# Optimization experiments

Measured on AMD Instinct MI355X. Metric: run time of the kernel, lower is better.

The kernel has to match this reference:

```python
import jax, jax.numpy as jnp
import numpy as np

BN_EPS = 1e-5


def _bn(x, gamma, beta):
    # training-mode BatchNorm1d: biased batch stats over the edge/batch axis
    mean = jnp.mean(x, axis=0, keepdims=True)
    var = jnp.mean((x - mean) ** 2, axis=0, keepdims=True)
    return (x - mean) * jax.lax.rsqrt(var + BN_EPS) * gamma + beta


def setup_inputs() -> dict:
    key = jax.random.key(0)
    ks = jax.random.split(key, 20)
    N, E = 20000, 300000
    in_drug, in_prot, hidden = 256, 512, 256
    h2 = 2 * hidden

    def u(k, shape, fan_in):
        b = 1.0 / np.sqrt(fan_in)
        return jax.random.uniform(k, shape, jnp.float32, -b, b)

    return {
        "x_drug": jax.random.normal(ks[0], (N, in_drug), jnp.float32),
        "x_prot": jax.random.normal(ks[1], (N, in_prot), jnp.float32),
        "edge_index": jax.random.randint(ks[2], (2, E), 0, N, jnp.int64),
        "W_src": u(ks[3], (hidden, in_drug), in_drug),
        "W_dst": u(ks[4], (hidden, in_prot), in_prot),
        "W_gate": u(ks[5], (h2, h2), h2),
        "b_gate": u(ks[6], (h2,), h2),
        "W1": u(ks[7], (hidden, h2), h2),
        "b1": u(ks[8], (hidden,), h2),
        "g1": jnp.ones((hidden,), jnp.float32),
        "be1": jnp.zeros((hidden,), jnp.float32),
        "W2": u(ks[9], (hidden, hidden), hidden),
        "b2": u(ks[10], (hidden,), hidden),
        "g2": jnp.ones((hidden,), jnp.float32),
        "be2": jnp.zeros((hidden,), jnp.float32),
        "W3": u(ks[11], (1, hidden), hidden),
        "b3": u(ks[12], (1,), hidden),
        "W_bil": u(ks[13], (1, hidden, hidden), hidden),
        "b_bil": u(ks[14], (1,), hidden),
    }


def reference(x_drug, x_prot, edge_index, W_src, W_dst, W_gate, b_gate,
              W1, b1, g1, be1, W2, b2, g2, be2, W3, b3, W_bil, b_bil):
    src, dst = edge_index[0], edge_index[1]
    h_src = x_drug[src] @ W_src.T            # [E, H]
    h_dst = x_prot[dst] @ W_dst.T            # [E, H]
    h_cat = jnp.concatenate([h_src, h_dst], axis=1)  # [E, 2H]
    gate = jax.nn.sigmoid(h_cat @ W_gate.T + b_gate)
    h = gate * h_cat
    # MLP (dropout is identity here)
    h1 = jax.nn.relu(_bn(h @ W1.T + b1, g1, be1))
    h2_ = jax.nn.relu(_bn(h1 @ W2.T + b2, g2, be2))
    mlp_score = (h2_ @ W3.T + b3).reshape(-1)
    # Bilinear: out_ek = sum_ij h_src_ei W_kij h_dst_ej + b_k
    bil_score = (jnp.einsum("ei,kij,ej->ek", h_src, W_bil, h_dst) + b_bil).reshape(-1)
    return mlp_score + bil_score
```

## Files before the change

kernel.cpp:

```cpp
#include <hip/hip_runtime.h>
#include <hip/hip_bf16.h>

typedef unsigned short u16;
typedef __attribute__((ext_vector_type(8))) short bf16x8;
typedef __attribute__((ext_vector_type(8))) unsigned short us8;
typedef __attribute__((ext_vector_type(4))) float f32x4;


__device__ __forceinline__ float b2f(u16 u) {
    union { unsigned u32; float f; } x; x.u32 = ((unsigned)u) << 16; return x.f;
}
__device__ __forceinline__ u16 f2b(float f) {
    union { float f; unsigned u; } x; x.f = f;
    unsigned r = x.u + 0x7fffu + ((x.u >> 16) & 1u);
    return (u16)(r >> 16);
}

__global__ __launch_bounds__(256) void zero_kernel(float* p, int n) {
    int i = blockIdx.x * 256 + threadIdx.x;
    if (i < n) p[i] = 0.f;
}

__global__ __launch_bounds__(256) void cvt_kernel(const float* __restrict__ in,
                                                  u16* __restrict__ out, int n4) {
    int i = blockIdx.x * 256 + threadIdx.x;
    const int stride = gridDim.x * 256;
    for (; i < n4; i += stride) {
        float4 v = ((const float4*)in)[i];
        ushort4 o; o.x = f2b(v.x); o.y = f2b(v.y); o.z = f2b(v.z); o.w = f2b(v.w);
        ((ushort4*)out)[i] = o;
    }
}

#define OP_PLAIN  0
#define OP_GATE   1
#define OP_BNRELU 2

template <int AOP, bool STATS, bool BIAS>
__global__ __launch_bounds__(256, 2) void mfma_gemm(
    const u16* __restrict__ Ain, int lda,
    const u16* __restrict__ Wb, int ldb,
    u16* __restrict__ C, int ldc,
    int M, int K,
    const int* __restrict__ ei, int E,
    const u16* __restrict__ Gs, const u16* __restrict__ Gd,
    const u16* __restrict__ Hs, const u16* __restrict__ Hd,
    const float* __restrict__ scaleK, const float* __restrict__ shiftK,
    const float* __restrict__ bias,
    float* __restrict__ sums)
{
    __shared__ u16 As[128][72];
    __shared__ u16 Bs[256][72];
    __shared__ float wsum[2][2][256];
    __shared__ int sx[128], dx[128];

    const int t = threadIdx.x;
    const int row0 = blockIdx.x * 128;
    const int col0 = blockIdx.y * 256;

    if constexpr (AOP == OP_GATE) {
        if (t < 128) {
            const int e = min(row0 + t, M - 1);
            sx[t] = ei[e]; dx[t] = ei[E + e];
        }
        __syncthreads();
    }

    const int arow = t >> 1;
    const int ks = (t & 1) * 32;
    const int agr = min(row0 + arow, M - 1);

    const int w = t >> 6, lane = t & 63;
    const int wr = w >> 1, wc = w & 1;
    const int lrow = lane & 15, lkg = lane >> 4;

    f32x4 acc[4][8] = {};

    for (int k0 = 0; k0 < K; k0 += 64) {
        {
            const u16* wp = Wb + (size_t)(col0 + t) * ldb + k0;
#pragma unroll
            for (int q = 0; q < 8; ++q)
                *(us8*)&Bs[t][q * 8] = *(const us8*)(wp + q * 8);
        }
        if constexpr (AOP == OP_PLAIN) {
            const u16* ap = Ain + (size_t)agr * lda + k0 + ks;
#pragma unroll
            for (int q = 0; q < 4; ++q)
                *(us8*)&As[arow][ks + q * 8] = *(const us8*)(ap + q * 8);
        } else if constexpr (AOP == OP_GATE) {
            const int s = sx[arow], d = dx[arow];
            const u16* gsp = Gs + (size_t)s * 512 + k0 + ks;
            const u16* gdp = Gd + (size_t)d * 512 + k0 + ks;
            const u16* hp = (k0 < 256) ? (Hs + (size_t)s * 256 + k0 + ks)
                                       : (Hd + (size_t)d * 256 + (k0 - 256) + ks);
#pragma unroll
            for (int q = 0; q < 4; ++q) {
                us8 g8 = *(const us8*)(gsp + q * 8);
                us8 d8 = *(const us8*)(gdp + q * 8);
                us8 h8 = *(const us8*)(hp + q * 8);
                us8 o;
#pragma unroll
                for (int j = 0; j < 8; ++j) {
                    const float x = b2f(g8[j]) + b2f(d8[j]);
                    const float g = 1.f / (1.f + __expf(-x));
                    o[j] = f2b(g * b2f(h8[j]));
                }
                *(us8*)&As[arow][ks + q * 8] = o;
            }
        } else {
            const u16* ap = Ain + (size_t)agr * lda + k0 + ks;
#pragma unroll
            for (int q = 0; q < 4; ++q) {
                us8 a8 = *(const us8*)(ap + q * 8);
                us8 o;
#pragma unroll
                for (int j = 0; j < 8; ++j) {
                    const int k = k0 + ks + q * 8 + j;
                    o[j] = f2b(fmaxf(fmaf(b2f(a8[j]), scaleK[k], shiftK[k]), 0.f));
                }
                *(us8*)&As[arow][ks + q * 8] = o;
            }
        }
        __syncthreads();
#pragma unroll
        for (int kk = 0; kk < 64; kk += 32) {
            bf16x8 af[4];
#pragma unroll
            for (int mi = 0; mi < 4; ++mi)
                af[mi] = *(const bf16x8*)&As[wr * 64 + mi * 16 + lrow][kk + lkg * 8];
#pragma unroll
            for (int ni = 0; ni < 8; ++ni) {
                bf16x8 bfr = *(const bf16x8*)&Bs[wc * 128 + ni * 16 + lrow][kk + lkg * 8];
#pragma unroll
                for (int mi = 0; mi < 4; ++mi)
                    acc[mi][ni] = __builtin_amdgcn_mfma_f32_16x16x32_bf16(
                        af[mi], bfr, acc[mi][ni], 0, 0, 0);
            }
        }
        __syncthreads();
    }

#pragma unroll
    for (int ni = 0; ni < 8; ++ni) {
        const int gcol = col0 + wc * 128 + ni * 16 + lrow;
        const float bv = BIAS ? bias[gcol] : 0.f;
        float s = 0.f, ss = 0.f;
#pragma unroll
        for (int mi = 0; mi < 4; ++mi) {
            f32x4 v = acc[mi][ni];
#pragma unroll
            for (int j = 0; j < 4; ++j) {
                const int grow = row0 + wr * 64 + mi * 16 + lkg * 4 + j;
                const float x = v[j] + bv;
                if (grow < M) {
                    C[(size_t)grow * ldc + gcol] = f2b(x);
                    if (STATS) { s += x; ss = fmaf(x, x, ss); }
                }
            }
        }
        if constexpr (STATS) {
            s  += __shfl_xor(s, 16, 64);  s  += __shfl_xor(s, 32, 64);
            ss += __shfl_xor(ss, 16, 64); ss += __shfl_xor(ss, 32, 64);
            if (lkg == 0) {
                wsum[0][wr][wc * 128 + ni * 16 + lrow] = s;
                wsum[1][wr][wc * 128 + ni * 16 + lrow] = ss;
            }
        }
    }
    if constexpr (STATS) {
        __syncthreads();
        atomicAdd(&sums[t],       wsum[0][0][t] + wsum[0][1][t]);
        atomicAdd(&sums[256 + t], wsum[1][0][t] + wsum[1][1][t]);
    }
}

__global__ void finalize_kernel(
    const float* __restrict__ sums, const float* __restrict__ g,
    const float* __restrict__ be, int M,
    float* __restrict__ scale, float* __restrict__ shift)
{
    const int c = threadIdx.x;
    const float inv = 1.f / (float)M;
    const float mean = sums[c] * inv;
    const float var  = sums[256 + c] * inv - mean * mean;
    const float sc = g[c] * rsqrtf(var + 1e-5f);
    scale[c] = sc;
    shift[c] = fmaf(-mean, sc, be[c]);
}

__global__ __launch_bounds__(256) void final_kernel(
    const u16* __restrict__ Z2,
    const float* __restrict__ scale2, const float* __restrict__ shift2,
    const float* __restrict__ W3, const float* __restrict__ b3,
    const int* __restrict__ ei,
    const u16* __restrict__ Hs, const u16* __restrict__ Bd,
    const float* __restrict__ b_bil,
    float* __restrict__ out, int E)
{
    const int w = threadIdx.x >> 6, lane = threadIdx.x & 63;
    const int e = blockIdx.x * 4 + w;
    if (e >= E) return;
    const int s = ei[e], d = ei[E + e];
    ushort4 zv = *(const ushort4*)(Z2 + (size_t)e * 256 + lane * 4);
    ushort4 hv = *(const ushort4*)(Hs + (size_t)s * 256 + lane * 4);
    ushort4 bv = *(const ushort4*)(Bd + (size_t)d * 256 + lane * 4);
    float4 sc = *(const float4*)(scale2 + lane * 4);
    float4 sh = *(const float4*)(shift2 + lane * 4);
    float4 w3 = *(const float4*)(W3 + lane * 4);
    const u16 zq[4] = {zv.x, zv.y, zv.z, zv.w};
    const u16 hq[4] = {hv.x, hv.y, hv.z, hv.w};
    const u16 bq[4] = {bv.x, bv.y, bv.z, bv.w};
    const float scq[4] = {sc.x, sc.y, sc.z, sc.w};
    const float shq[4] = {sh.x, sh.y, sh.z, sh.w};
    const float wq[4] = {w3.x, w3.y, w3.z, w3.w};
    float acc = 0.f;
#pragma unroll
    for (int i = 0; i < 4; ++i) {
        const float x = fmaxf(fmaf(b2f(zq[i]), scq[i], shq[i]), 0.f);
        acc = fmaf(x, wq[i], acc);
        acc = fmaf(b2f(hq[i]), b2f(bq[i]), acc);
    }
#pragma unroll
    for (int off = 32; off; off >>= 1) acc += __shfl_down(acc, off, 64);
    if (lane == 0) out[e] = acc + b3[0] + b_bil[0];
}

extern "C" void kernel_launch(void* const* d_in, const int* in_sizes, int n_in,
                              void* d_out, int out_size, void* d_ws, size_t ws_size,
                              hipStream_t stream)
{
    const float* x_drug = (const float*)d_in[0];
    const float* x_prot = (const float*)d_in[1];
    const int*   ei     = (const int*)d_in[2];
    const float* W_src  = (const float*)d_in[3];
    const float* W_dst  = (const float*)d_in[4];
    const float* W_gate = (const float*)d_in[5];
    const float* b_gate = (const float*)d_in[6];
    const float* W1     = (const float*)d_in[7];
    const float* g1     = (const float*)d_in[9];
    const float* be1    = (const float*)d_in[10];
    const float* W2     = (const float*)d_in[11];
    const float* g2     = (const float*)d_in[13];
    const float* be2    = (const float*)d_in[14];
    const float* W3     = (const float*)d_in[15];
    const float* b3     = (const float*)d_in[16];
    const float* W_bil  = (const float*)d_in[17];
    const float* b_bil  = (const float*)d_in[18];
    float* out = (float*)d_out;

    const int N = in_sizes[0] / 256;
    const int E = in_sizes[2] / 2;

    char* wp_ = (char*)d_ws;
    auto alloc = [&](size_t bytes) {
        char* p = wp_; wp_ += (bytes + 255) & ~(size_t)255; return p;
    };
    u16* xdb    = (u16*)alloc((size_t)N * 256 * 2);
    u16* xpb    = (u16*)alloc((size_t)N * 512 * 2);
    u16* Wsrcb  = (u16*)alloc(256 * 256 * 2);
    u16* Wdstb  = (u16*)alloc(256 * 512 * 2);
    u16* Wgateb = (u16*)alloc(512 * 512 * 2);
    u16* Wbilb  = (u16*)alloc(256 * 256 * 2);
    u16* W1b    = (u16*)alloc(256 * 512 * 2);
    u16* W2b    = (u16*)alloc(256 * 256 * 2);
    u16* Hs     = (u16*)alloc((size_t)N * 256 * 2);
    u16* Hd     = (u16*)alloc((size_t)N * 256 * 2);
    u16* Gs     = (u16*)alloc((size_t)N * 512 * 2);
    u16* Gd     = (u16*)alloc((size_t)N * 512 * 2);
    u16* Bd     = (u16*)alloc((size_t)N * 256 * 2);
    u16* z      = (u16*)alloc((size_t)E * 256 * 2);
    float* sums   = (float*)alloc(1024 * 4);
    float* scale1 = (float*)alloc(256 * 4);
    float* shift1 = (float*)alloc(256 * 4);
    float* scale2 = (float*)alloc(256 * 4);
    float* shift2 = (float*)alloc(256 * 4);

    zero_kernel<<<4, 256, 0, stream>>>(sums, 1024);

    auto cvt = [&](const float* in, u16* o, int n) {
        const int n4 = n / 4;
        cvt_kernel<<<min((n4 + 255) / 256, 2048), 256, 0, stream>>>(in, o, n4);
    };
    cvt(x_drug, xdb, N * 256);
    cvt(x_prot, xpb, N * 512);
    cvt(W_src,  Wsrcb,  256 * 256);
    cvt(W_dst,  Wdstb,  256 * 512);
    cvt(W_gate, Wgateb, 512 * 512);
    cvt(W_bil,  Wbilb,  256 * 256);
    cvt(W1,     W1b,    256 * 512);
    cvt(W2,     W2b,    256 * 256);

    const int mbN = (N + 127) / 128;
    const int mbE = (E + 127) / 128;

#define NULLS nullptr, 0, nullptr, nullptr, nullptr, nullptr
    mfma_gemm<OP_PLAIN, false, false><<<dim3(mbN, 1), 256, 0, stream>>>(
        xdb, 256, Wsrcb, 256, Hs, 256, N, 256, NULLS, nullptr, nullptr, nullptr, nullptr);
    mfma_gemm<OP_PLAIN, false, false><<<dim3(mbN, 1), 256, 0, stream>>>(
        xpb, 512, Wdstb, 512, Hd, 256, N, 512, NULLS, nullptr, nullptr, nullptr, nullptr);
    mfma_gemm<OP_PLAIN, false, true><<<dim3(mbN, 2), 256, 0, stream>>>(
        Hs, 256, Wgateb, 512, Gs, 512, N, 256, NULLS, nullptr, nullptr, b_gate, nullptr);
    mfma_gemm<OP_PLAIN, false, false><<<dim3(mbN, 2), 256, 0, stream>>>(
        Hd, 256, Wgateb + 256, 512, Gd, 512, N, 256, NULLS, nullptr, nullptr, nullptr, nullptr);
    mfma_gemm<OP_PLAIN, false, false><<<dim3(mbN, 1), 256, 0, stream>>>(
        Hd, 256, Wbilb, 256, Bd, 256, N, 256, NULLS, nullptr, nullptr, nullptr, nullptr);

    mfma_gemm<OP_GATE, true, false><<<dim3(mbE, 1), 256, 0, stream>>>(
        nullptr, 0, W1b, 512, z, 256, E, 512,
        ei, E, Gs, Gd, Hs, Hd, nullptr, nullptr, nullptr, sums);
    finalize_kernel<<<1, 256, 0, stream>>>(sums, g1, be1, E, scale1, shift1);

    mfma_gemm<OP_BNRELU, true, false><<<dim3(mbE, 1), 256, 0, stream>>>(
        z, 256, W2b, 256, z, 256, E, 256,
        NULLS, scale1, shift1, nullptr, sums + 512);
    finalize_kernel<<<1, 256, 0, stream>>>(sums + 512, g2, be2, E, scale2, shift2);

    final_kernel<<<(E + 3) / 4, 256, 0, stream>>>(
        z, scale2, shift2, W3, b3, ei, Hs, Bd, b_bil, out, E);
#undef NULLS
}
```

Before: 636.6 us.

## Double-buffer GEMM tiles, batch node GEMMs, fuse input casts and bilinear dot

```diff
diff --git a/kernel.cpp b/kernel.cpp
--- a/kernel.cpp
+++ b/kernel.cpp
@@ -21,158 +21,285 @@
     if (i < n) p[i] = 0.f;
 }
 
-__global__ __launch_bounds__(256) void cvt_kernel(const float* __restrict__ in,
-                                                  u16* __restrict__ out, int n4) {
+struct CvtSeg { const float* in; u16* out; int n4; };
+struct CvtArr { CvtSeg s[6]; int tot4; };
+__global__ __launch_bounds__(256) void cvt_fused(CvtArr ca) {
     int i = blockIdx.x * 256 + threadIdx.x;
-    const int stride = gridDim.x * 256;
-    for (; i < n4; i += stride) {
-        float4 v = ((const float4*)in)[i];
-        ushort4 o; o.x = f2b(v.x); o.y = f2b(v.y); o.z = f2b(v.z); o.w = f2b(v.w);
-        ((ushort4*)out)[i] = o;
-    }
-}
-
-#define OP_PLAIN  0
-#define OP_GATE   1
-#define OP_BNRELU 2
-
-template <int AOP, bool STATS, bool BIAS>
-__global__ __launch_bounds__(256, 2) void mfma_gemm(
-    const u16* __restrict__ Ain, int lda,
-    const u16* __restrict__ Wb, int ldb,
-    u16* __restrict__ C, int ldc,
-    int M, int K,
-    const int* __restrict__ ei, int E,
-    const u16* __restrict__ Gs, const u16* __restrict__ Gd,
-    const u16* __restrict__ Hs, const u16* __restrict__ Hd,
-    const float* __restrict__ scaleK, const float* __restrict__ shiftK,
-    const float* __restrict__ bias,
-    float* __restrict__ sums)
+    if (i >= ca.tot4) return;
+    int k = 0, off = i;
+#pragma unroll
+    for (int q = 0; q < 6; ++q) {
+        if (off < ca.s[q].n4) { k = q; break; }
+        off -= ca.s[q].n4;
+    }
+    float4 v = ((const float4*)ca.s[k].in)[off];
+    ushort4 o; o.x = f2b(v.x); o.y = f2b(v.y); o.z = f2b(v.z); o.w = f2b(v.w);
+    ((ushort4*)ca.s[k].out)[off] = o;
+}
+
+struct GDesc {
+    const void* A; int lda; int a_f32;
+    const u16* W; int ldb;
+    u16* C; int ldc;
+    int K;
+    const float* bias;
+};
+template <int NY> struct GDescArr { GDesc d[NY]; };
+
+template <int NY>
+__global__ __launch_bounds__(256, 2) void mfma_node(GDescArr<NY> da, int M)
 {
-    __shared__ u16 As[128][72];
-    __shared__ u16 Bs[256][72];
-    __shared__ float wsum[2][2][256];
-    __shared__ int sx[128], dx[128];
-
+    const GDesc dd = da.d[blockIdx.y];
+    __shared__ u16 As[2][128][40];
+    __shared__ u16 Bs[2][256][40];
     const int t = threadIdx.x;
     const int row0 = blockIdx.x * 128;
-    const int col0 = blockIdx.y * 256;
-
-    if constexpr (AOP == OP_GATE) {
-        if (t < 128) {
-            const int e = min(row0 + t, M - 1);
-            sx[t] = ei[e]; dx[t] = ei[E + e];
-        }
-        __syncthreads();
-    }
-
-    const int arow = t >> 1;
-    const int ks = (t & 1) * 32;
+    const int arow = t >> 1, aks = (t & 1) * 16;
     const int agr = min(row0 + arow, M - 1);
-
     const int w = t >> 6, lane = t & 63;
     const int wr = w >> 1, wc = w & 1;
     const int lrow = lane & 15, lkg = lane >> 4;
+    const int NIT = dd.K >> 5;
 
     f32x4 acc[4][8] = {};
-
-    for (int k0 = 0; k0 < K; k0 += 64) {
-        {
-            const u16* wp = Wb + (size_t)(col0 + t) * ldb + k0;
-#pragma unroll
-            for (int q = 0; q < 8; ++q)
-                *(us8*)&Bs[t][q * 8] = *(const us8*)(wp + q * 8);
-        }
-        if constexpr (AOP == OP_PLAIN) {
-            const u16* ap = Ain + (size_t)agr * lda + k0 + ks;
-#pragma unroll
-            for (int q = 0; q < 4; ++q)
-                *(us8*)&As[arow][ks + q * 8] = *(const us8*)(ap + q * 8);
-        } else if constexpr (AOP == OP_GATE) {
-            const int s = sx[arow], d = dx[arow];
-            const u16* gsp = Gs + (size_t)s * 512 + k0 + ks;
-            const u16* gdp = Gd + (size_t)d * 512 + k0 + ks;
-            const u16* hp = (k0 < 256) ? (Hs + (size_t)s * 256 + k0 + ks)
-                                       : (Hd + (size_t)d * 256 + (k0 - 256) + ks);
-#pragma unroll
-            for (int q = 0; q < 4; ++q) {
-                us8 g8 = *(const us8*)(gsp + q * 8);
-                us8 d8 = *(const us8*)(gdp + q * 8);
-                us8 h8 = *(const us8*)(hp + q * 8);
+    us8 ar[2], br[4];
+    float4 fr[4];
+
+    auto load_regs = [&](int it) {
+        const int k0 = it << 5;
+        if (dd.a_f32) {
+            const float* ap = (const float*)dd.A + (size_t)agr * dd.lda + k0 + aks;
+#pragma unroll
+            for (int q = 0; q < 4; ++q) fr[q] = *(const float4*)(ap + q * 4);
+        } else {
+            const u16* ap = (const u16*)dd.A + (size_t)agr * dd.lda + k0 + aks;
+            ar[0] = *(const us8*)ap; ar[1] = *(const us8*)(ap + 8);
+        }
+        const u16* wp = dd.W + (size_t)t * dd.ldb + k0;
+#pragma unroll
+        for (int q = 0; q < 4; ++q) br[q] = *(const us8*)(wp + q * 8);
+    };
+    auto proc_write = [&](int b) {
+        if (dd.a_f32) {
+#pragma unroll
+            for (int q = 0; q < 2; ++q) {
                 us8 o;
-#pragma unroll
-                for (int j = 0; j < 8; ++j) {
-                    const float x = b2f(g8[j]) + b2f(d8[j]);
-                    const float g = 1.f / (1.f + __expf(-x));
-                    o[j] = f2b(g * b2f(h8[j]));
-                }
-                *(us8*)&As[arow][ks + q * 8] = o;
+                const float fq[8] = {fr[q*2].x, fr[q*2].y, fr[q*2].z, fr[q*2].w,
+                                     fr[q*2+1].x, fr[q*2+1].y, fr[q*2+1].z, fr[q*2+1].w};
+#pragma unroll
+                for (int j = 0; j < 8; ++j) o[j] = f2b(fq[j]);
+                *(us8*)&As[b][arow][aks + q * 8] = o;
             }
         } else {
-            const u16* ap = Ain + (size_t)agr * lda + k0 + ks;
-#pragma unroll
-            for (int q = 0; q < 4; ++q) {
-                us8 a8 = *(const us8*)(ap + q * 8);
-                us8 o;
-#pragma unroll
-                for (int j = 0; j < 8; ++j) {
-                    const int k = k0 + ks + q * 8 + j;
-                    o[j] = f2b(fmaxf(fmaf(b2f(a8[j]), scaleK[k], shiftK[k]), 0.f));
-                }
-                *(us8*)&As[arow][ks + q * 8] = o;
-            }
-        }
+            *(us8*)&As[b][arow][aks] = ar[0];
+            *(us8*)&As[b][arow][aks + 8] = ar[1];
+        }
+#pragma unroll
+        for (int q = 0; q < 4; ++q) *(us8*)&Bs[b][t][q * 8] = br[q];
+    };
+    auto do_mfma = [&](int b) {
+        bf16x8 af[4];
+#pragma unroll
+        for (int mi = 0; mi < 4; ++mi)
+            af[mi] = *(const bf16x8*)&As[b][wr * 64 + mi * 16 + lrow][lkg * 8];
+#pragma unroll
+        for (int ni = 0; ni < 8; ++ni) {
+            bf16x8 bfr = *(const bf16x8*)&Bs[b][wc * 128 + ni * 16 + lrow][lkg * 8];
+#pragma unroll
+            for (int mi = 0; mi < 4; ++mi)
+                acc[mi][ni] = __builtin_amdgcn_mfma_f32_16x16x32_bf16(
+                    af[mi], bfr, acc[mi][ni], 0, 0, 0);
+        }
+    };
+
+    load_regs(0); proc_write(0); __syncthreads();
+    for (int it = 0; it < NIT; ++it) {
+        const int cur = it & 1;
+        if (it + 1 < NIT) load_regs(it + 1);
+        do_mfma(cur);
+        if (it + 1 < NIT) proc_write(cur ^ 1);
         __syncthreads();
-#pragma unroll
-        for (int kk = 0; kk < 64; kk += 32) {
-            bf16x8 af[4];
-#pragma unroll
-            for (int mi = 0; mi < 4; ++mi)
-                af[mi] = *(const bf16x8*)&As[wr * 64 + mi * 16 + lrow][kk + lkg * 8];
-#pragma unroll
-            for (int ni = 0; ni < 8; ++ni) {
-                bf16x8 bfr = *(const bf16x8*)&Bs[wc * 128 + ni * 16 + lrow][kk + lkg * 8];
-#pragma unroll
-                for (int mi = 0; mi < 4; ++mi)
-                    acc[mi][ni] = __builtin_amdgcn_mfma_f32_16x16x32_bf16(
-                        af[mi], bfr, acc[mi][ni], 0, 0, 0);
-            }
-        }
-        __syncthreads();
     }
 
 #pragma unroll
     for (int ni = 0; ni < 8; ++ni) {
-        const int gcol = col0 + wc * 128 + ni * 16 + lrow;
-        const float bv = BIAS ? bias[gcol] : 0.f;
-        float s = 0.f, ss = 0.f;
+        const int gcol = wc * 128 + ni * 16 + lrow;
+        const float bv = dd.bias ? dd.bias[gcol] : 0.f;
 #pragma unroll
         for (int mi = 0; mi < 4; ++mi) {
             f32x4 v = acc[mi][ni];
 #pragma unroll
             for (int j = 0; j < 4; ++j) {
                 const int grow = row0 + wr * 64 + mi * 16 + lkg * 4 + j;
-                const float x = v[j] + bv;
-                if (grow < M) {
-                    C[(size_t)grow * ldc + gcol] = f2b(x);
-                    if (STATS) { s += x; ss = fmaf(x, x, ss); }
+                if (grow < M) dd.C[(size_t)grow * dd.ldc + gcol] = f2b(v[j] + bv);
+            }
+        }
+    }
+}
+
+#define OP_GATE   1
+#define OP_BNRELU 2
+
+template <int AOP>
+__global__ __launch_bounds__(256, 2) void mfma_edge(
+    const u16* __restrict__ Ain,
+    const u16* __restrict__ Wb, int ldb, int K,
+    u16* __restrict__ C, int E,
+    const int* __restrict__ ei,
+    const u16* __restrict__ Gs, const u16* __restrict__ Gd,
+    const u16* __restrict__ Hs, const u16* __restrict__ Hd,
+    const u16* __restrict__ Bd, const float* __restrict__ b_bil,
+    float* __restrict__ bil,
+    const float* __restrict__ scaleK, const float* __restrict__ shiftK,
+    float* __restrict__ sums)
+{
+    __shared__ u16 As[2][128][40];
+    __shared__ u16 Bs[2][256][40];
+    __shared__ float wsum[2][2][256];
+    __shared__ int sx[128], dx[128];
+
+    const int t = threadIdx.x;
+    const int row0 = blockIdx.x * 128;
+
+    if constexpr (AOP == OP_GATE) {
+        if (t < 128) {
+            const int e = min(row0 + t, E - 1);
+            sx[t] = ei[e]; dx[t] = ei[E + e];
+        }
+        __syncthreads();
+    }
+
+    const int arow = t >> 1, aks = (t & 1) * 16;
+    const int agr = min(row0 + arow, E - 1);
+    const int w = t >> 6, lane = t & 63;
+    const int wr = w >> 1, wc = w & 1;
+    const int lrow = lane & 15, lkg = lane >> 4;
+    const int NIT = K >> 5;
+
+    f32x4 acc[4][8] = {};
+    float bdot = 0.f;
+    us8 g1r[2], g2r[2], hr[2], bdr[2], br[4];
+    float4 scA[2], scB[2], shA[2], shB[2];
+
+    auto load_regs = [&](int it) {
+        const int k0 = it << 5;
+        const int kg = k0 + aks;
+        if constexpr (AOP == OP_GATE) {
+            const int s = sx[arow], d = dx[arow];
+            const u16* gsp = Gs + (size_t)s * 512 + kg;
+            const u16* gdp = Gd + (size_t)d * 512 + kg;
+            g1r[0] = *(const us8*)gsp; g1r[1] = *(const us8*)(gsp + 8);
+            g2r[0] = *(const us8*)gdp; g2r[1] = *(const us8*)(gdp + 8);
+            const u16* hp = (k0 < 256) ? (Hs + (size_t)s * 256 + kg)
+                                       : (Hd + (size_t)d * 256 + kg - 256);
+            hr[0] = *(const us8*)hp; hr[1] = *(const us8*)(hp + 8);
+            if (k0 < 256) {
+                const u16* bp = Bd + (size_t)dx[arow] * 256 + kg;
+                bdr[0] = *(const us8*)bp; bdr[1] = *(const us8*)(bp + 8);
+            }
+        } else {
+            const u16* ap = Ain + (size_t)agr * 256 + kg;
+            g1r[0] = *(const us8*)ap; g1r[1] = *(const us8*)(ap + 8);
+#pragma unroll
+            for (int q = 0; q < 2; ++q) {
+                scA[q] = *(const float4*)(scaleK + kg + q * 8);
+                scB[q] = *(const float4*)(scaleK + kg + q * 8 + 4);
+                shA[q] = *(const float4*)(shiftK + kg + q * 8);
+                shB[q] = *(const float4*)(shiftK + kg + q * 8 + 4);
+            }
+        }
+        const u16* wp = Wb + (size_t)t * ldb + k0;
+#pragma unroll
+        for (int q = 0; q < 4; ++q) br[q] = *(const us8*)(wp + q * 8);
+    };
+    auto proc_write = [&](int it, int b) {
+        const int k0 = it << 5;
+#pragma unroll
+        for (int q = 0; q < 2; ++q) {
+            us8 o;
+            if constexpr (AOP == OP_GATE) {
+#pragma unroll
+                for (int j = 0; j < 8; ++j) {
+                    const float x = b2f(g1r[q][j]) + b2f(g2r[q][j]);
+                    const float g = 1.f / (1.f + __expf(-x));
+                    o[j] = f2b(g * b2f(hr[q][j]));
                 }
-            }
-        }
-        if constexpr (STATS) {
-            s  += __shfl_xor(s, 16, 64);  s  += __shfl_xor(s, 32, 64);
-            ss += __shfl_xor(ss, 16, 64); ss += __shfl_xor(ss, 32, 64);
-            if (lkg == 0) {
-                wsum[0][wr][wc * 128 + ni * 16 + lrow] = s;
-                wsum[1][wr][wc * 128 + ni * 16 + lrow] = ss;
-            }
-        }
-    }
-    if constexpr (STATS) {
+                if (k0 < 256) {
+#pragma unroll
+                    for (int j = 0; j < 8; ++j)
+                        bdot = fmaf(b2f(hr[q][j]), b2f(bdr[q][j]), bdot);
+                }
+            } else {
+                const float scq[8] = {scA[q].x, scA[q].y, scA[q].z, scA[q].w,
+                                      scB[q].x, scB[q].y, scB[q].z, scB[q].w};
+                const float shq[8] = {shA[q].x, shA[q].y, shA[q].z, shA[q].w,
+                                      shB[q].x, shB[q].y, shB[q].z, shB[q].w};
+#pragma unroll
+                for (int j = 0; j < 8; ++j)
+                    o[j] = f2b(fmaxf(fmaf(b2f(g1r[q][j]), scq[j], shq[j]), 0.f));
+            }
+            *(us8*)&As[b][arow][aks + q * 8] = o;
+        }
+#pragma unroll
+        for (int q = 0; q < 4; ++q) *(us8*)&Bs[b][t][q * 8] = br[q];
+    };
+    auto do_mfma = [&](int b) {
+        bf16x8 af[4];
+#pragma unroll
+        for (int mi = 0; mi < 4; ++mi)
+            af[mi] = *(const bf16x8*)&As[b][wr * 64 + mi * 16 + lrow][lkg * 8];
+#pragma unroll
+        for (int ni = 0; ni < 8; ++ni) {
+            bf16x8 bfr = *(const bf16x8*)&Bs[b][wc * 128 + ni * 16 + lrow][lkg * 8];
+#pragma unroll
+            for (int mi = 0; mi < 4; ++mi)
+                acc[mi][ni] = __builtin_amdgcn_mfma_f32_16x16x32_bf16(
+                    af[mi], bfr, acc[mi][ni], 0, 0, 0);
+        }
+    };
+
+    load_regs(0); proc_write(0, 0); __syncthreads();
+    for (int it = 0; it < NIT; ++it) {
+        const int cur = it & 1;
+        if (it + 1 < NIT) load_regs(it + 1);
+        do_mfma(cur);
+        if (it + 1 < NIT) proc_write(it + 1, cur ^ 1);
         __syncthreads();
-        atomicAdd(&sums[t],       wsum[0][0][t] + wsum[0][1][t]);
-        atomicAdd(&sums[256 + t], wsum[1][0][t] + wsum[1][1][t]);
-    }
+    }
+
+    if constexpr (AOP == OP_GATE) {
+        bdot += __shfl_xor(bdot, 1, 64);
+        if ((t & 1) == 0 && row0 + arow < E)
+            bil[row0 + arow] = bdot + b_bil[0];
+    }
+
+#pragma unroll
+    for (int ni = 0; ni < 8; ++ni) {
+        const int gcol = wc * 128 + ni * 16 + lrow;
+        float s = 0.f, ss = 0.f;
+#pragma unroll
+        for (int mi = 0; mi < 4; ++mi) {
+            f32x4 v = acc[mi][ni];
+#pragma unroll
+            for (int j = 0; j < 4; ++j) {
+                const int grow = row0 + wr * 64 + mi * 16 + lkg * 4 + j;
+                const float x = v[j];
+                if (grow < E) {
+                    C[(size_t)grow * 256 + gcol] = f2b(x);
+                    s += x; ss = fmaf(x, x, ss);
+                }
+            }
+        }
+        s  += __shfl_xor(s, 16, 64);  s  += __shfl_xor(s, 32, 64);
+        ss += __shfl_xor(ss, 16, 64); ss += __shfl_xor(ss, 32, 64);
+        if (lkg == 0) {
+            wsum[0][wr][gcol] = s;
+            wsum[1][wr][gcol] = ss;
+        }
+    }
+    __syncthreads();
+    atomicAdd(&sums[t],       wsum[0][0][t] + wsum[0][1][t]);
+    atomicAdd(&sums[256 + t], wsum[1][0][t] + wsum[1][1][t]);
 }
 
 __global__ void finalize_kernel(
@@ -193,24 +320,17 @@
     const u16* __restrict__ Z2,
     const float* __restrict__ scale2, const float* __restrict__ shift2,
     const float* __restrict__ W3, const float* __restrict__ b3,
-    const int* __restrict__ ei,
-    const u16* __restrict__ Hs, const u16* __restrict__ Bd,
-    const float* __restrict__ b_bil,
+    const float* __restrict__ bil,
     float* __restrict__ out, int E)
 {
     const int w = threadIdx.x >> 6, lane = threadIdx.x & 63;
     const int e = blockIdx.x * 4 + w;
     if (e >= E) return;
-    const int s = ei[e], d = ei[E + e];
     ushort4 zv = *(const ushort4*)(Z2 + (size_t)e * 256 + lane * 4);
-    ushort4 hv = *(const ushort4*)(Hs + (size_t)s * 256 + lane * 4);
-    ushort4 bv = *(const ushort4*)(Bd + (size_t)d * 256 + lane * 4);
     float4 sc = *(const float4*)(scale2 + lane * 4);
     float4 sh = *(const float4*)(shift2 + lane * 4);
     float4 w3 = *(const float4*)(W3 + lane * 4);
     const u16 zq[4] = {zv.x, zv.y, zv.z, zv.w};
-    const u16 hq[4] = {hv.x, hv.y, hv.z, hv.w};
-    const u16 bq[4] = {bv.x, bv.y, bv.z, bv.w};
     const float scq[4] = {sc.x, sc.y, sc.z, sc.w};
     const float shq[4] = {sh.x, sh.y, sh.z, sh.w};
     const float wq[4] = {w3.x, w3.y, w3.z, w3.w};
@@ -219,11 +339,10 @@
     for (int i = 0; i < 4; ++i) {
         const float x = fmaxf(fmaf(b2f(zq[i]), scq[i], shq[i]), 0.f);
         acc = fmaf(x, wq[i], acc);
-        acc = fmaf(b2f(hq[i]), b2f(bq[i]), acc);
     }
 #pragma unroll
     for (int off = 32; off; off >>= 1) acc += __shfl_down(acc, off, 64);
-    if (lane == 0) out[e] = acc + b3[0] + b_bil[0];
+    if (lane == 0) out[e] = acc + b3[0] + bil[e];
 }
 
 extern "C" void kernel_launch(void* const* d_in, const int* in_sizes, int n_in,
@@ -256,8 +375,6 @@
     auto alloc = [&](size_t bytes) {
         char* p = wp_; wp_ += (bytes + 255) & ~(size_t)255; return p;
     };
-    u16* xdb    = (u16*)alloc((size_t)N * 256 * 2);
-    u16* xpb    = (u16*)alloc((size_t)N * 512 * 2);
     u16* Wsrcb  = (u16*)alloc(256 * 256 * 2);
     u16* Wdstb  = (u16*)alloc(256 * 512 * 2);
     u16* Wgateb = (u16*)alloc(512 * 512 * 2);
@@ -270,6 +387,7 @@
     u16* Gd     = (u16*)alloc((size_t)N * 512 * 2);
     u16* Bd     = (u16*)alloc((size_t)N * 256 * 2);
     u16* z      = (u16*)alloc((size_t)E * 256 * 2);
+    float* bil  = (float*)alloc((size_t)E * 4);
     float* sums   = (float*)alloc(1024 * 4);
     float* scale1 = (float*)alloc(256 * 4);
     float* shift1 = (float*)alloc(256 * 4);
@@ -278,45 +396,44 @@
 
     zero_kernel<<<4, 256, 0, stream>>>(sums, 1024);
 
-    auto cvt = [&](const float* in, u16* o, int n) {
-        const int n4 = n / 4;
-        cvt_kernel<<<min((n4 + 255) / 256, 2048), 256, 0, stream>>>(in, o, n4);
-    };
-    cvt(x_drug, xdb, N * 256);
-    cvt(x_prot, xpb, N * 512);
-    cvt(W_src,  Wsrcb,  256 * 256);
-    cvt(W_dst,  Wdstb,  256 * 512);
-    cvt(W_gate, Wgateb, 512 * 512);
-    cvt(W_bil,  Wbilb,  256 * 256);
-    cvt(W1,     W1b,    256 * 512);
-    cvt(W2,     W2b,    256 * 256);
-
-    const int mbN = (N + 127) / 128;
-    const int mbE = (E + 127) / 128;
-
-#define NULLS nullptr, 0, nullptr, nullptr, nullptr, nullptr
-    mfma_gemm<OP_PLAIN, false, false><<<dim3(mbN, 1), 256, 0, stream>>>(
-        xdb, 256, Wsrcb, 256, Hs, 256, N, 256, NULLS, nullptr, nullptr, nullptr, nullptr);
-    mfma_gemm<OP_PLAIN, false, false><<<dim3(mbN, 1), 256, 0, stream>>>(
-        xpb, 512, Wdstb, 512, Hd, 256, N, 512, NULLS, nullptr, nullptr, nullptr, nullptr);
-    mfma_gemm<OP_PLAIN, false, true><<<dim3(mbN, 2), 256, 0, stream>>>(
-        Hs, 256, Wgateb, 512, Gs, 512, N, 256, NULLS, nullptr, nullptr, b_gate, nullptr);
-    mfma_gemm<OP_PLAIN, false, false><<<dim3(mbN, 2), 256, 0, stream>>>(
-        Hd, 256, Wgateb + 256, 512, Gd, 512, N, 256, NULLS, nullptr, nullptr, nullptr, nullptr);
-    mfma_gemm<OP_PLAIN, false, false><<<dim3(mbN, 1), 256, 0, stream>>>(
-        Hd, 256, Wbilb, 256, Bd, 256, N, 256, NULLS, nullptr, nullptr, nullptr, nullptr);
-
-    mfma_gemm<OP_GATE, true, false><<<dim3(mbE, 1), 256, 0, stream>>>(
-        nullptr, 0, W1b, 512, z, 256, E, 512,
-        ei, E, Gs, Gd, Hs, Hd, nullptr, nullptr, nullptr, sums);
+    CvtArr ca;
+    ca.s[0] = {W_src,  Wsrcb,  256 * 256 / 4};
+    ca.s[1] = {W_dst,  Wdstb,  256 * 512 / 4};
+    ca.s[2] = {W_gate, Wgateb, 512 * 512 / 4};
+    ca.s[3] = {W_bil,  Wbilb,  256 * 256 / 4};
+    ca.s[4] = {W1,     W1b,    256 * 512 / 4};
+    ca.s[5] = {W2,     W2b,    256 * 256 / 4};
+    ca.tot4 = 0;
+    for (int q = 0; q < 6; ++q) ca.tot4 += ca.s[q].n4;
+    cvt_fused<<<(ca.tot4 + 255) / 256, 256, 0, stream>>>(ca);
+
+    const int gxN = (N + 127) / 128;
+    const int gxE = (E + 127) / 128;
+
+    GDescArr<2> p1;
+    p1.d[0] = {x_drug, 256, 1, Wsrcb, 256, Hs, 256, 256, nullptr};
+    p1.d[1] = {x_prot, 512, 1, Wdstb, 512, Hd, 256, 512, nullptr};
+    mfma_node<2><<<dim3(gxN, 2), 256, 0, stream>>>(p1, N);
+
+    GDescArr<5> p2;
+    p2.d[0] = {Hs, 256, 0, Wgateb,                 512, Gs,       512, 256, b_gate};
+    p2.d[1] = {Hs, 256, 0, Wgateb + 256 * 512,     512, Gs + 256, 512, 256, b_gate + 256};
+    p2.d[2] = {Hd, 256, 0, Wgateb + 256,           512, Gd,       512, 256, nullptr};
+    p2.d[3] = {Hd, 256, 0, Wgateb + 256 * 512 + 256, 512, Gd + 256, 512, 256, nullptr};
+    p2.d[4] = {Hd, 256, 0, Wbilb,                  256, Bd,       256, 256, nullptr};
+    mfma_node<5><<<dim3(gxN, 5), 256, 0, stream>>>(p2, N);
+
+    mfma_edge<OP_GATE><<<gxE, 256, 0, stream>>>(
+        nullptr, W1b, 512, 512, z, E,
+        ei, Gs, Gd, Hs, Hd, Bd, b_bil, bil, nullptr, nullptr, sums);
     finalize_kernel<<<1, 256, 0, stream>>>(sums, g1, be1, E, scale1, shift1);
 
-    mfma_gemm<OP_BNRELU, true, false><<<dim3(mbE, 1), 256, 0, stream>>>(
-        z, 256, W2b, 256, z, 256, E, 256,
-        NULLS, scale1, shift1, nullptr, sums + 512);
+    mfma_edge<OP_BNRELU><<<gxE, 256, 0, stream>>>(
+        z, W2b, 256, 256, z, E,
+        nullptr, nullptr, nullptr, nullptr, nullptr, nullptr, nullptr, nullptr,
+        scale1, shift1, sums + 512);
     finalize_kernel<<<1, 256, 0, stream>>>(sums + 512, g2, be2, E, scale2, shift2);
 
     final_kernel<<<(E + 3) / 4, 256, 0, stream>>>(
-        z, scale2, shift2, W3, b3, ei, Hs, Bd, b_bil, out, E);
-#undef NULLS
-}
+        z, scale2, shift2, W3, b3, bil, out, E);
+}
```

After: 588.9 us. 1.08x faster.
